# Optimization experiments

Hardware: AMD Instinct MI355X
Metric: run time of the kernel (lower is better)

Reference implementation:

```python
import jax, jax.numpy as jnp
import numpy as np

B = 16; Hp = 24; Wp = 24; N = Hp * Wp + 2  # 578 = patches + cls + freq tokens
D = 768; H = 12; HDIM = D // H
BAND = 64; SD = 16  # sd = min(16, max(4, band_dim))
HID = 3072  # int(embed_dim * mlp_ratio)
SCALE = HDIM ** -0.5; CLIP = 10.0
FILM_SCALE = 0.5; SPEC_INIT = 0.02; GATE_INIT = 0.05


def _ln(x, w, b, eps=1e-6):
    m = jnp.mean(x, axis=-1, keepdims=True)
    v = jnp.mean((x - m) ** 2, axis=-1, keepdims=True)
    return (x - m) * jax.lax.rsqrt(v + eps) * w + b


def _rms(x, eps=1e-6):
    return x * jax.lax.rsqrt(jnp.mean(x * x, axis=-1, keepdims=True) + eps)


def setup_inputs() -> dict:
    key = jax.random.key(0)
    ks = jax.random.split(key, 16)
    rn = lambda k, s, sc=1.0: jax.random.normal(k, s, dtype=jnp.float32) * sc
    return {
        "x": rn(ks[0], (B, N, D)),
        "band_tokens": rn(ks[1], (B, 1, D)),  # unused by forward (matches torch signature)
        "freq_token_for_cond": rn(ks[2], (B, 1, D)),
        "freq_summary": rn(ks[3], (B, D)),
        "token_band_feat": rn(ks[4], (B, N, BAND)),
        "alpha": jnp.ones((1,), jnp.float32),
        "ln_gate_w": jnp.ones((D,), jnp.float32), "ln_gate_b": jnp.zeros((D,), jnp.float32),
        "film_w": rn(ks[5], (D, 2 * D), 1e-4), "film_b": jnp.zeros((2 * D,), jnp.float32),
        "ln_attn_w": jnp.ones((D,), jnp.float32), "ln_attn_b": jnp.zeros((D,), jnp.float32),
        "qkv_w": rn(ks[6], (D, 3 * D), 0.02), "qkv_b": jnp.zeros((3 * D,), jnp.float32),
        "proj_w": rn(ks[7], (D, D), 0.02), "proj_b": jnp.zeros((D,), jnp.float32),
        "spec_bias_scale": jnp.float32(SPEC_INIT),
        "gate_w": rn(ks[8], (D, H), 1e-4), "gate_b": jnp.zeros((H,), jnp.float32),
        "band_proj_w": rn(ks[9], (BAND, SD), 0.02),
        "ln_mlp_w": jnp.ones((D,), jnp.float32), "ln_mlp_b": jnp.zeros((D,), jnp.float32),
        "fc1_w": rn(ks[10], (D, HID), 0.02), "fc1_b": jnp.zeros((HID,), jnp.float32),
        "fc2_w": rn(ks[11], (HID, D), 0.02), "fc2_b": jnp.zeros((D,), jnp.float32),
        "dw_w": rn(ks[12], (HID, 1, 3, 3), 0.1), "dw_b": jnp.zeros((HID,), jnp.float32),
    }


def _forward(x, band_tokens, freq_token_for_cond, freq_summary, token_band_feat, alpha,
             ln_gate_w, ln_gate_b, film_w, film_b, ln_attn_w, ln_attn_b,
             qkv_w, qkv_b, proj_w, proj_b, spec_bias_scale, gate_w, gate_b, band_proj_w,
             ln_mlp_w, ln_mlp_b, fc1_w, fc1_b, fc2_w, fc2_b, dw_w, dw_b):
    a = alpha.reshape(())
    # --- FiLM gate on patch tokens (replaces patch, no residual) ---
    cls_freq = x[:, :2]
    patch = x[:, 2:]
    p = _ln(patch, ln_gate_w, ln_gate_b)
    gb = freq_summary @ film_w + film_b            # [B, 2D]
    gamma, beta = jnp.split(gb, 2, axis=-1)
    gamma = jnp.tanh(gamma) * FILM_SCALE
    beta = jnp.tanh(beta) * FILM_SCALE
    patch = p * (1.0 + a * gamma[:, None, :]) + a * beta[:, None, :]
    x = jnp.concatenate([cls_freq, patch], axis=1)
    # --- spectral-similarity attention ---
    xn = _ln(x, ln_attn_w, ln_attn_b)
    qkv = (xn @ qkv_w + qkv_b).reshape(B, N, 3, H, HDIM)
    q = _rms(qkv[:, :, 0].transpose(0, 2, 1, 3))   # [B,H,N,hd]
    k = _rms(qkv[:, :, 1].transpose(0, 2, 1, 3))
    v = qkv[:, :, 2].transpose(0, 2, 1, 3)
    logits = jnp.einsum('bhnd,bhmd->bhnm', q * SCALE, k)
    s = _rms(token_band_feat @ band_proj_w)        # [B,N,SD]
    ssim = jnp.einsum('bns,bms->bnm', s, s)        # [B,N,N]
    logits = jnp.clip(logits + a * spec_bias_scale * ssim[:, None], -CLIP, CLIP)
    attn = jax.nn.softmax(logits, axis=-1)
    out = jnp.einsum('bhnm,bhmd->bhnd', attn, v)
    g = jnp.tanh(freq_token_for_cond[:, 0] @ gate_w + gate_b) * GATE_INIT  # [B,H]
    out = out * (1.0 + a * g[:, :, None, None])
    out = out.transpose(0, 2, 1, 3).reshape(B, N, D)
    x = x + (out @ proj_w + proj_b)
    # --- conv MLP on patch tokens only ---
    cls_freq = x[:, :2]
    patch = x[:, 2:]
    h = jax.nn.gelu(_ln(patch, ln_mlp_w, ln_mlp_b) @ fc1_w + fc1_b, approximate=False)
    h = h.transpose(0, 2, 1).reshape(B, HID, Hp, Wp)
    h = jax.lax.conv_general_dilated(h, dw_w, (1, 1), 'SAME', feature_group_count=HID,
                                     dimension_numbers=('NCHW', 'OIHW', 'NCHW'))
    h = jax.nn.silu(h + dw_b[None, :, None, None])
    h = h.reshape(B, HID, Hp * Wp).transpose(0, 2, 1)
    patch = patch + (h @ fc2_w + fc2_b)
    return jnp.concatenate([cls_freq, patch], axis=1)


def reference(x, band_tokens, freq_token_for_cond, freq_summary, token_band_feat, alpha,
              ln_gate_w, ln_gate_b, film_w, film_b, ln_attn_w, ln_attn_b,
              qkv_w, qkv_b, proj_w, proj_b, spec_bias_scale, gate_w, gate_b, band_proj_w,
              ln_mlp_w, ln_mlp_b, fc1_w, fc1_b, fc2_w, fc2_b, dw_w, dw_b):
    return _forward(x, band_tokens, freq_token_for_cond, freq_summary, token_band_feat, alpha,
                    ln_gate_w, ln_gate_b, film_w, film_b, ln_attn_w, ln_attn_b,
                    qkv_w, qkv_b, proj_w, proj_b, spec_bias_scale, gate_w, gate_b, band_proj_w,
                    ln_mlp_w, ln_mlp_b, fc1_w, fc1_b, fc2_w, fc2_b, dw_w, dw_b)
```

## Files before the change

### kernel.cpp

```cpp
#include <hip/hip_runtime.h>
#include <hip/hip_bf16.h>

#define BATCH 16
#define NTOK 578
#define NTOKP 592
#define NP 576
#define PGRID 24
#define DIM 768
#define NH 12
#define HDIM 64
#define BAND 64
#define SDIM 16
#define HID 3072
#define SCALE 0.125f
#define CLIPV 10.0f
#define KHS 104
#define VTS 72
#define PLS 72
#define FKS 16

typedef __attribute__((ext_vector_type(8))) short bf16x8;
typedef __attribute__((ext_vector_type(4))) float f32x4;

__device__ __forceinline__ float b2f(short u) {
  union { float f; unsigned int i; } x;
  x.i = ((unsigned int)(unsigned short)u) << 16;
  return x.f;
}
__device__ __forceinline__ short f2b(float x) {
  __hip_bfloat16 h = __float2bfloat16(x);
  return *reinterpret_cast<short*>(&h);
}

__device__ __forceinline__ void gload16(const short* g, short* l) {
  __builtin_amdgcn_global_load_lds(
      (const __attribute__((address_space(1))) unsigned int*)g,
      (__attribute__((address_space(3))) unsigned int*)l, 16, 0, 0);
}

__device__ __forceinline__ int swz_wgid(int orig, int nwg) {
  int xcd = orig & 7, i = orig >> 3;
  int q = nwg >> 3, r = nwg & 7;
  return (xcd < r) ? xcd * (q + 1) + i : r * (q + 1) + (xcd - r) * q + i;
}

__device__ __forceinline__ void block_reduce2(float& a, float& b) {
  __shared__ float sm[8];
  #pragma unroll
  for (int o = 32; o > 0; o >>= 1) { a += __shfl_down(a, o); b += __shfl_down(b, o); }
  int lane = threadIdx.x & 63, w = threadIdx.x >> 6;
  __syncthreads();
  if (lane == 0) { sm[w] = a; sm[4 + w] = b; }
  __syncthreads();
  a = sm[0] + sm[1] + sm[2] + sm[3];
  b = sm[4] + sm[5] + sm[6] + sm[7];
}

#define TKS 266
__device__ __forceinline__ void tw2(
    const float* __restrict__ W, short* __restrict__ Wt, int K, int N,
    int kblk, int nblk, short* t) {
  int tid = threadIdx.x;
  int k0 = kblk * 256, n0 = nblk * 64;
  int r0 = tid >> 4, c0 = (tid & 15) * 4;
  #pragma unroll
  for (int it = 0; it < 16; it++) {
    int r = it * 16 + r0;
    float4 v = *(const float4*)(W + (size_t)(k0 + r) * N + n0 + c0);
    t[(c0 + 0) * TKS + r] = f2b(v.x);
    t[(c0 + 1) * TKS + r] = f2b(v.y);
    t[(c0 + 2) * TKS + r] = f2b(v.z);
    t[(c0 + 3) * TKS + r] = f2b(v.w);
  }
  __syncthreads();
  int n1 = tid >> 5, k1 = (tid & 31) * 8;
  #pragma unroll
  for (int it = 0; it < 8; it++) {
    int n = it * 8 + n1;
    *(bf16x8*)(Wt + (size_t)(n0 + n) * K + k0 + k1) = *(bf16x8*)(t + n * TKS + k1);
  }
}

__global__ __launch_bounds__(256) void prep_weights(
    const float* __restrict__ qkv_w, const float* __restrict__ proj_w,
    const float* __restrict__ fc1_w, const float* __restrict__ fc2_w,
    const float* __restrict__ dww,
    short* __restrict__ qkvT, short* __restrict__ projT,
    short* __restrict__ fc1T, short* __restrict__ fc2T, float* __restrict__ dwt) {
  __shared__ short t[64 * TKS];
  int id = blockIdx.x;
  if (id < 108) {
    tw2(qkv_w, qkvT, 768, 2304, id % 3, id / 3, t);
  } else if (id < 144) {
    int u = id - 108; tw2(proj_w, projT, 768, 768, u % 3, u / 3, t);
  } else if (id < 288) {
    int u = id - 144; tw2(fc1_w, fc1T, 768, 3072, u % 3, u / 3, t);
  } else if (id < 432) {
    int u = id - 288; tw2(fc2_w, fc2T, 3072, 768, u % 12, u / 12, t);
  } else {
    int i = (id - 432) * 256 + threadIdx.x;
    if (i < 9 * HID) { int tt = i / HID, c = i - tt * HID; dwt[i] = dww[c * 9 + tt]; }
  }
}

__global__ __launch_bounds__(256) void film_part(
    const float* __restrict__ fsum, const float* __restrict__ film_w,
    float* __restrict__ part) {
  __shared__ float fs[BATCH][48];
  int bid = blockIdx.x;
  int cg = bid % 12, ks = bid / 12;
  int tid = threadIdx.x;
  int k0 = ks * 48;
  for (int i = tid; i < BATCH * 48; i += 256) {
    int b = i / 48, kk = i - b * 48;
    fs[b][kk] = fsum[b * DIM + k0 + kk];
  }
  __syncthreads();
  int col4 = cg * 128 + (tid & 31) * 4;
  int bq = tid >> 5;
  float a0[4] = {0.f, 0.f, 0.f, 0.f}, a1[4] = {0.f, 0.f, 0.f, 0.f};
  #pragma unroll 4
  for (int kk = 0; kk < 48; kk++) {
    float4 w = *(const float4*)(film_w + (size_t)(k0 + kk) * 2 * DIM + col4);
    float f0 = fs[bq][kk], f1 = fs[bq + 8][kk];
    a0[0] += f0 * w.x; a0[1] += f0 * w.y; a0[2] += f0 * w.z; a0[3] += f0 * w.w;
    a1[0] += f1 * w.x; a1[1] += f1 * w.y; a1[2] += f1 * w.z; a1[3] += f1 * w.w;
  }
  *(float4*)(part + ((size_t)ks * BATCH + bq) * 1536 + col4) =
      (float4){a0[0], a0[1], a0[2], a0[3]};
  *(float4*)(part + ((size_t)ks * BATCH + bq + 8) * 1536 + col4) =
      (float4){a1[0], a1[1], a1[2], a1[3]};
}

__global__ __launch_bounds__(256) void film_fin(
    const float* __restrict__ part, const float* __restrict__ film_b,
    const float* __restrict__ ftc, const float* __restrict__ gate_w,
    const float* __restrict__ gate_b,
    float* __restrict__ gamma, float* __restrict__ beta, float* __restrict__ g) {
  int bid = blockIdx.x;
  if (bid < 96) {
    int idx = bid * 256 + threadIdx.x;
    int b = idx / 1536, col = idx - b * 1536;
    float acc = film_b[col];
    #pragma unroll
    for (int ks = 0; ks < FKS; ks++)
      acc += part[((size_t)ks * BATCH + b) * 1536 + col];
    float t = tanhf(acc) * 0.5f;
    if (col < DIM) gamma[b * DIM + col] = t;
    else beta[b * DIM + (col - DIM)] = t;
  } else {
    int widx = (bid - 96) * 4 + (threadIdx.x >> 6);
    int lane = threadIdx.x & 63;
    if (widx < BATCH * NH) {
      int b = widx / NH, h = widx - b * NH;
      float acc = 0.f;
      for (int kk = lane; kk < DIM; kk += 64) acc += ftc[b * DIM + kk] * gate_w[kk * NH + h];
      #pragma unroll
      for (int o = 32; o > 0; o >>= 1) acc += __shfl_down(acc, o);
      if (lane == 0) g[widx] = tanhf(acc + gate_b[h]) * 0.05f;
    }
  }
}

__global__ __launch_bounds__(256) void band_s_kernel(
    const float* __restrict__ tbf, const float* __restrict__ bw, float* __restrict__ s) {
  int row = blockIdx.x * 4 + (threadIdx.x >> 6);
  int lane = threadIdx.x & 63;
  if (row >= BATCH * NTOK) return;
  const float* t = tbf + (size_t)row * BAND;
  float val = 0.f;
  if (lane < SDIM) {
    for (int i = 0; i < BAND; i++) val += t[i] * bw[i * SDIM + lane];
  }
  float ss = val * val;
  #pragma unroll
  for (int o = 8; o > 0; o >>= 1) ss += __shfl_xor(ss, o, 16);
  if (lane < SDIM) s[(size_t)row * SDIM + lane] = val * rsqrtf(ss * (1.f / 16.f) + 1e-6f);
}

__global__ __launch_bounds__(256) void transpose_v(
    const short* __restrict__ v, short* __restrict__ vT) {
  __shared__ short t[64][72];
  int bh = blockIdx.y;
  int n0 = blockIdx.x * 64;
  int tid = threadIdx.x;
  const short* vb = v + (size_t)bh * NTOK * HDIM;
  short* ob = vT + (size_t)bh * HDIM * NTOKP;
  {
    int r = tid >> 2, c0 = (tid & 3) * 16;
    int n = n0 + r;
    bf16x8 a0 = {0,0,0,0,0,0,0,0}, a1 = {0,0,0,0,0,0,0,0};
    if (n < NTOK) {
      a0 = *(const bf16x8*)(vb + (size_t)n * HDIM + c0);
      a1 = *(const bf16x8*)(vb + (size_t)n * HDIM + c0 + 8);
    }
    *(bf16x8*)(&t[r][c0]) = a0;
    *(bf16x8*)(&t[r][c0 + 8]) = a1;
  }
  __syncthreads();
  {
    int d = tid & 63, nc = tid >> 6;
    int nbase = n0 + nc * 16;
    short tmp[16];
    #pragma unroll
    for (int e = 0; e < 16; e++) tmp[e] = t[nc * 16 + e][d];
    if (nbase + 16 <= NTOK) {
      *(bf16x8*)(ob + (size_t)d * NTOKP + nbase) = *(bf16x8*)tmp;
      *(bf16x8*)(ob + (size_t)d * NTOKP + nbase + 8) = *(bf16x8*)(tmp + 8);
    } else {
      for (int e = 0; e < 16; e++)
        if (nbase + e < NTOK) ob[(size_t)d * NTOKP + nbase + e] = tmp[e];
    }
  }
}

__global__ __launch_bounds__(256) void ln_film_kernel(
    const float* __restrict__ x, const float* __restrict__ gamma, const float* __restrict__ beta,
    const float* __restrict__ gw, const float* __restrict__ gb,
    const float* __restrict__ aw, const float* __restrict__ ab,
    const float* __restrict__ alpha, float* __restrict__ xw, __hip_bfloat16* __restrict__ xn) {
  int row = blockIdx.x;
  int b = row / NTOK, n = row % NTOK;
  int tid = threadIdx.x;
  const float* xr = x + (size_t)row * DIM;
  float vals[3];
  #pragma unroll
  for (int j = 0; j < 3; j++) vals[j] = xr[tid + j * 256];
  if (n >= 2) {
    float s = vals[0] + vals[1] + vals[2];
    float ss = vals[0]*vals[0] + vals[1]*vals[1] + vals[2]*vals[2];
    block_reduce2(s, ss);
    float mean = s * (1.f / 768.f);
    float inv = rsqrtf(ss * (1.f / 768.f) - mean * mean + 1e-6f);
    float a = alpha[0];
    #pragma unroll
    for (int j = 0; j < 3; j++) {
      int d = tid + j * 256;
      float p = (vals[j] - mean) * inv * gw[d] + gb[d];
      vals[j] = p * (1.f + a * gamma[(size_t)b * DIM + d]) + a * beta[(size_t)b * DIM + d];
    }
  }
  float* xwr = xw + (size_t)row * DIM;
  #pragma unroll
  for (int j = 0; j < 3; j++) xwr[tid + j * 256] = vals[j];
  float s = vals[0] + vals[1] + vals[2];
  float ss = vals[0]*vals[0] + vals[1]*vals[1] + vals[2]*vals[2];
  block_reduce2(s, ss);
  float mean = s * (1.f / 768.f);
  float inv = rsqrtf(ss * (1.f / 768.f) - mean * mean + 1e-6f);
  __hip_bfloat16* xnr = xn + (size_t)row * DIM;
  #pragma unroll
  for (int j = 0; j < 3; j++) {
    int d = tid + j * 256;
    xnr[d] = __float2bfloat16((vals[j] - mean) * inv * aw[d] + ab[d]);
  }
}

__device__ __forceinline__ void stage_tile256(
    const short* __restrict__ A, const short* __restrict__ Wt, int K,
    int m0, int n0, int kt, short* Al, short* Bl, int wid, int lrow, int lcolsw) {
  #pragma unroll
  for (int it = 0; it < 4; it++) {
    int r0 = wid * 8 + it * 64;
    gload16(A + (size_t)(m0 + r0 + lrow) * K + kt + lcolsw, Al + r0 * 64);
  }
  #pragma unroll
  for (int it = 0; it < 2; it++) {
    int r0 = wid * 8 + it * 64;
    gload16(Wt + (size_t)(n0 + r0 + lrow) * K + kt + lcolsw, Bl + r0 * 64);
  }
}

__device__ __forceinline__ void compute_tile256(
    const short* Al, const short* Bl, f32x4 acc[4][4],
    int wr, int wc, int ln15, int kb) {
  int rx = ln15 & 7;
  #pragma unroll
  for (int kk = 0; kk < 2; kk++) {
    int csw = ((kk * 4 + kb) ^ rx) * 8;
    bf16x8 af[4], bfr[4];
    #pragma unroll
    for (int i = 0; i < 4; i++)
      af[i] = *(const bf16x8*)(Al + (wr * 64 + i * 16 + ln15) * 64 + csw);
    #pragma unroll
    for (int j = 0; j < 4; j++)
      bfr[j] = *(const bf16x8*)(Bl + (wc * 64 + j * 16 + ln15) * 64 + csw);
    #pragma unroll
    for (int i = 0; i < 4; i++)
      #pragma unroll
      for (int j = 0; j < 4; j++)
        acc[i][j] = __builtin_amdgcn_mfma_f32_16x16x32_bf16(af[i], bfr[j], acc[i][j], 0, 0, 0);
  }
}

__device__ __forceinline__ void mfma_core_256(
    const short* __restrict__ A, const short* __restrict__ Wt,
    int K, int m0, int n0, f32x4 acc[4][4], short* Al, short* Bl) {
  int tid = threadIdx.x, lane = tid & 63, wid = tid >> 6;
  int wr = wid >> 1, wc = wid & 1;
  int ln15 = lane & 15, kb = lane >> 4;
  int lrow = lane >> 3;
  int lcolsw = (((lane & 7) ^ lrow) & 7) * 8;
  #pragma unroll
  for (int i = 0; i < 4; i++)
    #pragma unroll
    for (int j = 0; j < 4; j++) acc[i][j] = (f32x4){0.f, 0.f, 0.f, 0.f};
  for (int kt = 0; kt < K; kt += 64) {
    stage_tile256(A, Wt, K, m0, n0, kt, Al, Bl, wid, lrow, lcolsw);
    __syncthreads();
    compute_tile256(Al, Bl, acc, wr, wc, ln15, kb);
    __syncthreads();
  }
}

__device__ __forceinline__ void stage_tile64(
    const short* __restrict__ A, const short* __restrict__ Wt, int K,
    int m0, int n0, int kt, short* Al, short* Bl, int wid, int lrow, int lcolsw) {
  #pragma unroll
  for (int it = 0; it < 2; it++) {
    int r0 = wid * 8 + it * 32;
    gload16(A + (size_t)(m0 + r0 + lrow) * K + kt + lcolsw, Al + r0 * 64);
  }
  #pragma unroll
  for (int it = 0; it < 4; it++) {
    int r0 = wid * 8 + it * 32;
    gload16(Wt + (size_t)(n0 + r0 + lrow) * K + kt + lcolsw, Bl + r0 * 64);
  }
}

__device__ __forceinline__ void compute_tile64(
    const short* Al, const short* Bl, f32x4 acc[4][2],
    int wid, int ln15, int kb) {
  int rx = ln15 & 7;
  #pragma unroll
  for (int kk = 0; kk < 2; kk++) {
    int csw = ((kk * 4 + kb) ^ rx) * 8;
    bf16x8 af[4], bfr[2];
    #pragma unroll
    for (int i = 0; i < 4; i++)
      af[i] = *(const bf16x8*)(Al + (i * 16 + ln15) * 64 + csw);
    #pragma unroll
    for (int j = 0; j < 2; j++)
      bfr[j] = *(const bf16x8*)(Bl + (wid * 32 + j * 16 + ln15) * 64 + csw);
    #pragma unroll
    for (int i = 0; i < 4; i++)
      #pragma unroll
      for (int j = 0; j < 2; j++)
        acc[i][j] = __builtin_amdgcn_mfma_f32_16x16x32_bf16(af[i], bfr[j], acc[i][j], 0, 0, 0);
  }
}

__device__ __forceinline__ void mfma_core_64(
    const short* __restrict__ A, const short* __restrict__ Wt,
    int K, int m0, int n0, f32x4 acc[4][2],
    short* Al0, short* Bl0, short* Al1, short* Bl1) {
  int tid = threadIdx.x, lane = tid & 63, wid = tid >> 6;
  int ln15 = lane & 15, kb = lane >> 4;
  int lrow = lane >> 3;
  int lcolsw = (((lane & 7) ^ lrow) & 7) * 8;
  #pragma unroll
  for (int i = 0; i < 4; i++)
    #pragma unroll
    for (int j = 0; j < 2; j++) acc[i][j] = (f32x4){0.f, 0.f, 0.f, 0.f};
  stage_tile64(A, Wt, K, m0, n0, 0, Al0, Bl0, wid, lrow, lcolsw);
  __syncthreads();
  for (int kt = 0; kt < K; kt += 128) {
    if (kt + 64 < K)
      stage_tile64(A, Wt, K, m0, n0, kt + 64, Al1, Bl1, wid, lrow, lcolsw);
    compute_tile64(Al0, Bl0, acc, wid, ln15, kb);
    __syncthreads();
    if (kt + 128 < K)
      stage_tile64(A, Wt, K, m0, n0, kt + 128, Al0, Bl0, wid, lrow, lcolsw);
    if (kt + 64 < K)
      compute_tile64(Al1, Bl1, acc, wid, ln15, kb);
    __syncthreads();
  }
}

__global__ __launch_bounds__(512) void gemm_qkv(
    const short* __restrict__ A, const short* __restrict__ Wt, const float* __restrict__ bias,
    __hip_bfloat16* __restrict__ q, __hip_bfloat16* __restrict__ k, __hip_bfloat16* __restrict__ v) {
  __shared__ short Al[256 * 64], Bl[128 * 64];
  f32x4 acc[4][4];
  int wgid = swz_wgid(blockIdx.x, 37 * 18);
  int m0 = (wgid % 37) * 256, n0 = (wgid / 37) * 128;
  mfma_core_256(A, Wt, DIM, m0, n0, acc, Al, Bl);
  int tid = threadIdx.x, lane = tid & 63, wid = tid >> 6, wr = wid >> 1, wc = wid & 1;
  int ln15 = lane & 15, lq = lane >> 4;
  int colbase = n0 + wc * 64;
  int which = colbase / DIM;
  int rem = colbase - which * DIM;
  int h = rem >> 6;
  __hip_bfloat16* dst = (which == 0) ? q : ((which == 1) ? k : v);
  float fin_scale = (which == 0) ? SCALE : 1.0f;
  float bv[4];
  #pragma unroll
  for (int j = 0; j < 4; j++) bv[j] = bias[colbase + j * 16 + ln15];
  #pragma unroll
  for (int i = 0; i < 4; i++) {
    #pragma unroll
    for (int r = 0; r < 4; r++) {
      int m = m0 + wr * 64 + i * 16 + lq * 4 + r;
      float v4[4];
      #pragma unroll
      for (int j = 0; j < 4; j++) v4[j] = acc[i][j][r] + bv[j];
      float inv = fin_scale;
      if (which < 2) {
        float ss = v4[0]*v4[0] + v4[1]*v4[1] + v4[2]*v4[2] + v4[3]*v4[3];
        ss += __shfl_xor(ss, 1); ss += __shfl_xor(ss, 2);
        ss += __shfl_xor(ss, 4); ss += __shfl_xor(ss, 8);
        inv = rsqrtf(ss * (1.f / 64.f) + 1e-6f) * fin_scale;
      }
      if (m < BATCH * NTOK) {
        int b = m / NTOK, n = m - b * NTOK;
        __hip_bfloat16* orow = dst + (((size_t)b * NH + h) * NTOK + n) * HDIM;
        #pragma unroll
        for (int j = 0; j < 4; j++)
          orow[j * 16 + ln15] = __float2bfloat16(v4[j] * inv);
      }
    }
  }
}

__global__ __launch_bounds__(512) void attn_mfma(
    const short* __restrict__ q, const short* __restrict__ k,
    const short* __restrict__ vT, const float* __restrict__ s,
    const float* __restrict__ g, const float* __restrict__ alpha,
    const float* __restrict__ sbs, short* __restrict__ ao) {
  __shared__ short Kh[2][64 * KHS];
  __shared__ short Vt[2][64 * VTS];
  __shared__ short Pl[8][16 * PLS];
  int xcd = blockIdx.x & 7, idx = blockIdx.x >> 3;
  int bh = xcd * 24 + idx / 5;
  int n0 = (idx % 5) * 128;
  int b = bh / NH, h = bh - b * NH;
  int tid = threadIdx.x, lane = tid & 63, w = tid >> 6;
  int l15 = lane & 15, lg = lane >> 4;
  float a = alpha[0], c = a * sbs[0];
  const short* qb = q + (size_t)bh * NTOK * HDIM;
  const short* kb = k + (size_t)bh * NTOK * HDIM;
  const short* vtb = vT + (size_t)bh * HDIM * NTOKP;
  const float* sb = s + (size_t)b * NTOK * SDIM;
  const bf16x8 Z8 = {0, 0, 0, 0, 0, 0, 0, 0};

  int qrow = n0 + w * 16 + l15;
  int qsrc = (qrow < NTOK) ? qrow : 0;
  bf16x8 qf0 = *(const bf16x8*)(qb + (size_t)qsrc * HDIM + lg * 8);
  bf16x8 qf1 = *(const bf16x8*)(qb + (size_t)qsrc * HDIM + 32 + lg * 8);
  bf16x8 qf2 = Z8;
  if (lg < 2) {
    const float* sp = sb + (size_t)qsrc * SDIM + lg * 8;
    #pragma unroll
    for (int j = 0; j < 8; j++) qf2[j] = f2b(c * sp[j]);
  }

  f32x4 accO[4];
  #pragma unroll
  for (int dd = 0; dd < 4; dd++) accO[dd] = (f32x4){0.f, 0.f, 0.f, 0.f};
  float rsum[4] = {0.f, 0.f, 0.f, 0.f};

  int srow = (tid & 255) >> 2, sseg = tid & 3;
  if (tid < 256 && sseg == 3) {
    #pragma unroll
    for (int bb = 0; bb < 2; bb++) {
      short* dst = Kh[bb] + srow * KHS + 80;
      *(bf16x8*)dst = Z8;
      *(bf16x8*)(dst + 8) = Z8;
    }
  }

  auto stage = [&](int mt, short* KhB, short* VtB) {
    if (tid < 256) {
      int key = mt + srow;
      bool kok = key < NTOK;
      if (sseg < 2) {
        bf16x8 v0 = Z8, v1 = Z8, v2 = Z8, v3 = Z8;
        if (kok) {
          const short* src = kb + (size_t)key * HDIM + sseg * 32;
          v0 = *(const bf16x8*)(src);
          v1 = *(const bf16x8*)(src + 8);
          v2 = *(const bf16x8*)(src + 16);
          v3 = *(const bf16x8*)(src + 24);
        }
        short* dst = KhB + srow * KHS + sseg * 32;
        *(bf16x8*)dst = v0;
        *(bf16x8*)(dst + 8) = v1;
        *(bf16x8*)(dst + 16) = v2;
        *(bf16x8*)(dst + 24) = v3;
      } else if (sseg == 2) {
        bf16x8 v0 = Z8, v1 = Z8;
        if (kok) {
          const float* sp = sb + (size_t)key * SDIM;
          #pragma unroll
          for (int j = 0; j < 8; j++) { v0[j] = f2b(sp[j]); v1[j] = f2b(sp[j + 8]); }
        }
        short* dst = KhB + srow * KHS + 64;
        *(bf16x8*)dst = v0;
        *(bf16x8*)(dst + 8) = v1;
      }
    } else {
      int kk0 = sseg * 16;
      short* dst = VtB + srow * VTS + kk0;
      const short* src = vtb + (size_t)srow * NTOKP + mt + kk0;
      if (mt + kk0 + 16 <= NTOK) {
        *(bf16x8*)dst = *(const bf16x8*)src;
        *(bf16x8*)(dst + 8) = *(const bf16x8*)(src + 8);
      } else {
        for (int e = 0; e < 16; e++)
          dst[e] = (mt + kk0 + e < NTOK) ? src[e] : (short)0;
      }
    }
  };

  stage(0, Kh[0], Vt[0]);
  __syncthreads();
  const int NT = 10;
  for (int ti = 0; ti < NT; ti++) {
    int mt = ti * 64, cur = ti & 1;
    if (ti + 1 < NT) stage(mt + 64, Kh[cur ^ 1], Vt[cur ^ 1]);
    const short* KhC = Kh[cur];
    const short* VtC = Vt[cur];
    f32x4 sa[4];
    __builtin_amdgcn_s_setprio(1);
    #pragma unroll
    for (int jj = 0; jj < 4; jj++) {
      sa[jj] = (f32x4){0.f, 0.f, 0.f, 0.f};
      const short* kp = KhC + (jj * 16 + l15) * KHS + lg * 8;
      sa[jj] = __builtin_amdgcn_mfma_f32_16x16x32_bf16(qf0, *(const bf16x8*)kp, sa[jj], 0, 0, 0);
      sa[jj] = __builtin_amdgcn_mfma_f32_16x16x32_bf16(qf1, *(const bf16x8*)(kp + 32), sa[jj], 0, 0, 0);
      sa[jj] = __builtin_amdgcn_mfma_f32_16x16x32_bf16(qf2, *(const bf16x8*)(kp + 64), sa[jj], 0, 0, 0);
    }
    __builtin_amdgcn_s_setprio(0);
    short* pw = Pl[w];
    float ps[4][4];
    #pragma unroll
    for (int jj = 0; jj < 4; jj++) {
      bool ok = (mt + jj * 16 + l15) < NTOK;
      #pragma unroll
      for (int r = 0; r < 4; r++) {
        float x = sa[jj][r];
        x = fminf(fmaxf(x, -CLIPV), CLIPV);
        float e = ok ? __expf(x) : 0.f;
        ps[jj][r] = e;
        pw[(lg * 4 + r) * PLS + jj * 16 + l15] = f2b(e);
      }
    }
    #pragma unroll
    for (int r = 0; r < 4; r++) {
      float t = ps[0][r] + ps[1][r] + ps[2][r] + ps[3][r];
      t += __shfl_xor(t, 1); t += __shfl_xor(t, 2);
      t += __shfl_xor(t, 4); t += __shfl_xor(t, 8);
      rsum[r] += t;
    }
    __builtin_amdgcn_s_setprio(1);
    #pragma unroll
    for (int kc = 0; kc < 2; kc++) {
      bf16x8 pa = *(const bf16x8*)(pw + l15 * PLS + kc * 32 + lg * 8);
      #pragma unroll
      for (int dd = 0; dd < 4; dd++) {
        bf16x8 vf = *(const bf16x8*)(VtC + (dd * 16 + l15) * VTS + kc * 32 + lg * 8);
        accO[dd] = __builtin_amdgcn_mfma_f32_16x16x32_bf16(pa, vf, accO[dd], 0, 0, 0);
      }
    }
    __builtin_amdgcn_s_setprio(0);
    __syncthreads();
  }
  float gm = 1.f + a * g[bh];
  #pragma unroll
  for (int r = 0; r < 4; r++) {
    int n = n0 + w * 16 + lg * 4 + r;
    if (n >= NTOK) continue;
    float inv = gm / rsum[r];
    short* orow = ao + ((size_t)b * NTOK + n) * DIM + h * HDIM;
    #pragma unroll
    for (int dd = 0; dd < 4; dd++)
      orow[dd * 16 + l15] = f2b(accO[dd][r] * inv);
  }
}

__global__ __launch_bounds__(256) void gemm_proj(
    const short* __restrict__ A, const short* __restrict__ Wt, const float* __restrict__ bias,
    float* __restrict__ xw, float* __restrict__ out) {
  __shared__ short Al0[64 * 64], Bl0[128 * 64], Al1[64 * 64], Bl1[128 * 64];
  f32x4 acc[4][2];
  int wgid = swz_wgid(blockIdx.x, 145 * 6);
  int m0 = (wgid % 145) * 64, n0 = (wgid / 145) * 128;
  mfma_core_64(A, Wt, DIM, m0, n0, acc, Al0, Bl0, Al1, Bl1);
  int tid = threadIdx.x, lane = tid & 63, wid = tid >> 6;
  int ln15 = lane & 15, lq = lane >> 4;
  #pragma unroll
  for (int i = 0; i < 4; i++) {
    #pragma unroll
    for (int j = 0; j < 2; j++) {
      int col = n0 + wid * 32 + j * 16 + ln15;
      float bv = bias[col];
      #pragma unroll
      for (int r = 0; r < 4; r++) {
        int m = m0 + i * 16 + lq * 4 + r;
        if (m >= BATCH * NTOK) continue;
        int n = m % NTOK;
        float val = acc[i][j][r] + bv + xw[(size_t)m * DIM + col];
        xw[(size_t)m * DIM + col] = val;
        if (n < 2) out[(size_t)m * DIM + col] = val;
      }
    }
  }
}

__global__ __launch_bounds__(256) void ln_mlp_kernel(
    const float* __restrict__ x2, const float* __restrict__ w, const float* __restrict__ bb,
    __hip_bfloat16* __restrict__ xm) {
  int r = blockIdx.x;
  int b = r / NP, pi = r % NP;
  int tid = threadIdx.x;
  const float* xr = x2 + ((size_t)b * NTOK + 2 + pi) * DIM;
  float vals[3];
  #pragma unroll
  for (int j = 0; j < 3; j++) vals[j] = xr[tid + j * 256];
  float s = vals[0] + vals[1] + vals[2];
  float ss = vals[0]*vals[0] + vals[1]*vals[1] + vals[2]*vals[2];
  block_reduce2(s, ss);
  float mean = s * (1.f / 768.f);
  float inv = rsqrtf(ss * (1.f / 768.f) - mean * mean + 1e-6f);
  __hip_bfloat16* xo = xm + (size_t)r * DIM;
  #pragma unroll
  for (int j = 0; j < 3; j++) {
    int d = tid + j * 256;
    xo[d] = __float2bfloat16((vals[j] - mean) * inv * w[d] + bb[d]);
  }
}

__global__ __launch_bounds__(512) void gemm_fc1(
    const short* __restrict__ A, const short* __restrict__ Wt, const float* __restrict__ bias,
    __hip_bfloat16* __restrict__ h1) {
  __shared__ short Al[256 * 64], Bl[128 * 64];
  f32x4 acc[4][4];
  int wgid = swz_wgid(blockIdx.x, 18 * 24);
  int m0 = (wgid % 18) * 256, n0 = (wgid / 18) * 128;
  mfma_core_256(A, Wt, DIM, m0, n0, acc, Al, Bl);
  int tid = threadIdx.x, lane = tid & 63, wid = tid >> 6, wr = wid >> 1, wc = wid & 1;
  int ln15 = lane & 15, lq = lane >> 4;
  #pragma unroll
  for (int i = 0; i < 4; i++) {
    #pragma unroll
    for (int j = 0; j < 4; j++) {
      int col = n0 + wc * 64 + j * 16 + ln15;
      float bv = bias[col];
      #pragma unroll
      for (int r = 0; r < 4; r++) {
        int m = m0 + wr * 64 + i * 16 + lq * 4 + r;
        float val = acc[i][j][r] + bv;
        float ge = 0.5f * val * (1.f + erff(val * 0.70710678118f));
        h1[(size_t)m * HID + col] = __float2bfloat16(ge);
      }
    }
  }
}

__global__ __launch_bounds__(256) void dwconv_kernel(
    const __hip_bfloat16* __restrict__ h1, const float* __restrict__ dwt,
    const float* __restrict__ dwb, __hip_bfloat16* __restrict__ h2) {
  int gx = blockIdx.x;
  int b = gx / 144, g = gx - b * 144;
  int y = g / 6, x0 = (g - y * 6) * 4;
  int tid = threadIdx.x;
  int c0 = blockIdx.y * 512 + (tid & 63) * 8;
  int x = x0 + (tid >> 6);
  const short* in = (const short*)h1 + (size_t)b * NP * HID + c0;
  bf16x8 iv[3][3];
  #pragma unroll
  for (int ky = 0; ky < 3; ky++) {
    int yy = y + ky - 1;
    #pragma unroll
    for (int kx = 0; kx < 3; kx++) {
      int xx = x + kx - 1;
      bool ok = (yy >= 0 && yy < PGRID && xx >= 0 && xx < PGRID);
      iv[ky][kx] = ok ? *(const bf16x8*)(in + (size_t)(yy * PGRID + xx) * HID)
                      : (bf16x8){0, 0, 0, 0, 0, 0, 0, 0};
    }
  }
  float acc[8];
  {
    float4 b0 = *(const float4*)(dwb + c0);
    float4 b1 = *(const float4*)(dwb + c0 + 4);
    acc[0] = b0.x; acc[1] = b0.y; acc[2] = b0.z; acc[3] = b0.w;
    acc[4] = b1.x; acc[5] = b1.y; acc[6] = b1.z; acc[7] = b1.w;
  }
  #pragma unroll
  for (int t = 0; t < 9; t++) {
    float4 w0 = *(const float4*)(dwt + t * HID + c0);
    float4 w1 = *(const float4*)(dwt + t * HID + c0 + 4);
    bf16x8 xv = iv[t / 3][t % 3];
    acc[0] += b2f(xv[0]) * w0.x; acc[1] += b2f(xv[1]) * w0.y;
    acc[2] += b2f(xv[2]) * w0.z; acc[3] += b2f(xv[3]) * w0.w;
    acc[4] += b2f(xv[4]) * w1.x; acc[5] += b2f(xv[5]) * w1.y;
    acc[6] += b2f(xv[6]) * w1.z; acc[7] += b2f(xv[7]) * w1.w;
  }
  short ov[8];
  #pragma unroll
  for (int e = 0; e < 8; e++) {
    float v = acc[e];
    ov[e] = f2b(v / (1.f + __expf(-v)));
  }
  *(bf16x8*)((short*)h2 + ((size_t)b * NP + y * PGRID + x) * HID + c0) = *(bf16x8*)ov;
}

__global__ __launch_bounds__(256) void gemm_fc2(
    const short* __restrict__ A, const short* __restrict__ Wt, const float* __restrict__ bias,
    const float* __restrict__ xw, float* __restrict__ out, int b0) {
  __shared__ short Al0[64 * 64], Bl0[128 * 64], Al1[64 * 64], Bl1[128 * 64];
  f32x4 acc[4][2];
  int wgid = swz_wgid(blockIdx.x, 72 * 6);
  int m0 = (wgid % 72) * 64, n0 = (wgid / 72) * 128;
  mfma_core_64(A, Wt, HID, m0, n0, acc, Al0, Bl0, Al1, Bl1);
  int tid = threadIdx.x, lane = tid & 63, wid = tid >> 6;
  int ln15 = lane & 15, lq = lane >> 4;
  #pragma unroll
  for (int i = 0; i < 4; i++) {
    #pragma unroll
    for (int j = 0; j < 2; j++) {
      int col = n0 + wid * 32 + j * 16 + ln15;
      float bv = bias[col];
      #pragma unroll
      for (int r = 0; r < 4; r++) {
        int m = m0 + i * 16 + lq * 4 + r;
        int bl = m / NP, pi = m - bl * NP;
        size_t orow = ((size_t)(b0 + bl) * NTOK + 2 + pi) * DIM;
        out[orow + col] = acc[i][j][r] + bv + xw[orow + col];
      }
    }
  }
}

extern "C" void kernel_launch(void* const* d_in, const int* in_sizes, int n_in,
                              void* d_out, int out_size, void* d_ws, size_t ws_size,
                              hipStream_t stream) {
  const float* x      = (const float*)d_in[0];
  const float* ftc    = (const float*)d_in[2];
  const float* fsum   = (const float*)d_in[3];
  const float* tbf    = (const float*)d_in[4];
  const float* alpha  = (const float*)d_in[5];
  const float* lgw    = (const float*)d_in[6];
  const float* lgb    = (const float*)d_in[7];
  const float* film_w = (const float*)d_in[8];
  const float* film_b = (const float*)d_in[9];
  const float* law    = (const float*)d_in[10];
  const float* lab    = (const float*)d_in[11];
  const float* qkv_w  = (const float*)d_in[12];
  const float* qkv_b  = (const float*)d_in[13];
  const float* proj_w = (const float*)d_in[14];
  const float* proj_b = (const float*)d_in[15];
  const float* sbs    = (const float*)d_in[16];
  const float* gate_w = (const float*)d_in[17];
  const float* gate_b = (const float*)d_in[18];
  const float* band_w = (const float*)d_in[19];
  const float* lmw    = (const float*)d_in[20];
  const float* lmb    = (const float*)d_in[21];
  const float* fc1_w  = (const float*)d_in[22];
  const float* fc1_b  = (const float*)d_in[23];
  const float* fc2_w  = (const float*)d_in[24];
  const float* fc2_b  = (const float*)d_in[25];
  const float* dw_w   = (const float*)d_in[26];
  const float* dw_b   = (const float*)d_in[27];
  float* out = (float*)d_out;

  float* ws = (float*)d_ws;
  const size_t SZ = (size_t)BATCH * NTOK * DIM;

  float* p_xw = ws;
  short* p_xn = (short*)(ws + SZ);
  short* p_q  = (short*)(ws + SZ + SZ / 2);
  short* p_k  = (short*)(ws + 2 * SZ);
  short* p_v  = (short*)(ws + 2 * SZ + SZ / 2);
  float* p_s  = ws + 3 * SZ;
  float* p_gamma = p_s + (size_t)BATCH * NTOK * SDIM;
  float* p_beta  = p_gamma + BATCH * DIM;
  float* p_g     = p_beta + BATCH * DIM;
  float* p_dwt   = p_g + 256;
  float* p_part  = p_dwt + 9 * HID;
  float* wtb = p_part + (size_t)FKS * BATCH * 1536;
  short* qkvT = (short*)wtb;
  short* projT = qkvT + (size_t)768 * 2304;
  short* fc1T  = projT + (size_t)768 * 768;
  short* fc2T  = fc1T + (size_t)768 * 3072;
  short* h2c   = fc2T + (size_t)3072 * 768;

  const size_t total_floats =
      3 * SZ + (size_t)BATCH * NTOK * SDIM + 2 * (size_t)BATCH * DIM + 256 + 9 * HID +
      (size_t)FKS * BATCH * 1536 +
      ((size_t)768 * 2304 + 768 * 768 + 768 * 3072 + 3072 * 768) / 2 +
      ((size_t)8 * NP * HID) / 2;
  if (ws_size < total_floats * sizeof(float)) return;

  short* p_ao = p_xn;
  short* p_xm = p_q;
  short* h1c  = p_k;
  short* p_vT = h2c;

  dim3 blk(256);

  prep_weights<<<dim3(432 + 108), blk, 0, stream>>>(
      qkv_w, proj_w, fc1_w, fc2_w, dw_w, qkvT, projT, fc1T, fc2T, p_dwt);

  film_part<<<dim3(12 * FKS), blk, 0, stream>>>(fsum, film_w, p_part);

  film_fin<<<dim3(96 + 48), blk, 0, stream>>>(
      p_part, film_b, ftc, gate_w, gate_b, p_gamma, p_beta, p_g);

  band_s_kernel<<<dim3((BATCH * NTOK + 3) / 4), blk, 0, stream>>>(tbf, band_w, p_s);

  ln_film_kernel<<<dim3(BATCH * NTOK), blk, 0, stream>>>(
      x, p_gamma, p_beta, lgw, lgb, law, lab, alpha, p_xw, (__hip_bfloat16*)p_xn);

  gemm_qkv<<<dim3(37 * 18), dim3(512), 0, stream>>>(
      p_xn, qkvT, qkv_b, (__hip_bfloat16*)p_q, (__hip_bfloat16*)p_k, (__hip_bfloat16*)p_v);

  transpose_v<<<dim3(10, BATCH * NH), blk, 0, stream>>>(p_v, p_vT);

  attn_mfma<<<dim3(960), dim3(512), 0, stream>>>(
      p_q, p_k, p_vT, p_s, p_g, alpha, sbs, p_ao);

  gemm_proj<<<dim3(145 * 6), blk, 0, stream>>>(p_ao, projT, proj_b, p_xw, out);

  ln_mlp_kernel<<<dim3(BATCH * NP), blk, 0, stream>>>(p_xw, lmw, lmb, (__hip_bfloat16*)p_xm);

  for (int cc = 0; cc < 2; cc++) {
    const short* Ach = p_xm + (size_t)cc * 4608 * DIM;
    gemm_fc1<<<dim3(18 * 24), dim3(512), 0, stream>>>(Ach, fc1T, fc1_b, (__hip_bfloat16*)h1c);
    dwconv_kernel<<<dim3(8 * 144, 6), blk, 0, stream>>>(
        (const __hip_bfloat16*)h1c, p_dwt, dw_b, (__hip_bfloat16*)h2c);
    gemm_fc2<<<dim3(72 * 6), blk, 0, stream>>>(h2c, fc2T, fc2_b, p_xw, out, cc * 8);
  }
}
```

Measured before the change: 440.8 us.

## Pipeline 64-wide GEMM loads with vmcnt waits and single-buffer attention K tile

The 64-tile GEMM core now prefetches two K-tiles ahead. It uses raw s_barrier plus explicit s_waitcnt vmcnt counts instead of full __syncthreads, so global loads stay in flight across the barrier. The attention kernel drops the double-buffered K tile and uses one K buffer. A barrier is added after the QK MFMAs, after which the next K/V tile is staged, which lowers LDS use and may raise occupancy. The risks are that the hand-counted vmcnt values may not match the loads the compiler actually emits, and the extra barrier in attention serializes K staging against the score computation.

```diff
diff --git a/kernel.cpp b/kernel.cpp
--- a/kernel.cpp
+++ b/kernel.cpp
@@ -363,17 +363,24 @@
     #pragma unroll
     for (int j = 0; j < 2; j++) acc[i][j] = (f32x4){0.f, 0.f, 0.f, 0.f};
   stage_tile64(A, Wt, K, m0, n0, 0, Al0, Bl0, wid, lrow, lcolsw);
-  __syncthreads();
-  for (int kt = 0; kt < K; kt += 128) {
-    if (kt + 64 < K)
-      stage_tile64(A, Wt, K, m0, n0, kt + 64, Al1, Bl1, wid, lrow, lcolsw);
-    compute_tile64(Al0, Bl0, acc, wid, ln15, kb);
-    __syncthreads();
-    if (kt + 128 < K)
-      stage_tile64(A, Wt, K, m0, n0, kt + 128, Al0, Bl0, wid, lrow, lcolsw);
-    if (kt + 64 < K)
-      compute_tile64(Al1, Bl1, acc, wid, ln15, kb);
-    __syncthreads();
+  stage_tile64(A, Wt, K, m0, n0, 64, Al1, Bl1, wid, lrow, lcolsw);
+  asm volatile("s_waitcnt vmcnt(6)" ::: "memory");
+  __builtin_amdgcn_s_barrier();
+  const int NKT = K >> 6;
+  for (int t = 0; t < NKT; t++) {
+    const short* Ac = (t & 1) ? Al1 : Al0;
+    const short* Bc = (t & 1) ? Bl1 : Bl0;
+    compute_tile64(Ac, Bc, acc, wid, ln15, kb);
+    __builtin_amdgcn_s_barrier();
+    if (t + 2 < NKT) {
+      short* As = (t & 1) ? Al1 : Al0;
+      short* Bs = (t & 1) ? Bl1 : Bl0;
+      stage_tile64(A, Wt, K, m0, n0, (t + 2) << 6, As, Bs, wid, lrow, lcolsw);
+      asm volatile("s_waitcnt vmcnt(6)" ::: "memory");
+    } else if (t + 1 < NKT) {
+      asm volatile("s_waitcnt vmcnt(0)" ::: "memory");
+    }
+    __builtin_amdgcn_s_barrier();
   }
 }
 
@@ -427,7 +434,7 @@
     const short* __restrict__ vT, const float* __restrict__ s,
     const float* __restrict__ g, const float* __restrict__ alpha,
     const float* __restrict__ sbs, short* __restrict__ ao) {
-  __shared__ short Kh[2][64 * KHS];
+  __shared__ short Kh[64 * KHS];
   __shared__ short Vt[2][64 * VTS];
   __shared__ short Pl[8][16 * PLS];
   int xcd = blockIdx.x & 7, idx = blockIdx.x >> 3;
@@ -461,76 +468,75 @@
 
   int srow = (tid & 255) >> 2, sseg = tid & 3;
   if (tid < 256 && sseg == 3) {
-    #pragma unroll
-    for (int bb = 0; bb < 2; bb++) {
-      short* dst = Kh[bb] + srow * KHS + 80;
-      *(bf16x8*)dst = Z8;
-      *(bf16x8*)(dst + 8) = Z8;
-    }
-  }
-
-  auto stage = [&](int mt, short* KhB, short* VtB) {
-    if (tid < 256) {
-      int key = mt + srow;
-      bool kok = key < NTOK;
-      if (sseg < 2) {
-        bf16x8 v0 = Z8, v1 = Z8, v2 = Z8, v3 = Z8;
-        if (kok) {
-          const short* src = kb + (size_t)key * HDIM + sseg * 32;
-          v0 = *(const bf16x8*)(src);
-          v1 = *(const bf16x8*)(src + 8);
-          v2 = *(const bf16x8*)(src + 16);
-          v3 = *(const bf16x8*)(src + 24);
-        }
-        short* dst = KhB + srow * KHS + sseg * 32;
-        *(bf16x8*)dst = v0;
-        *(bf16x8*)(dst + 8) = v1;
-        *(bf16x8*)(dst + 16) = v2;
-        *(bf16x8*)(dst + 24) = v3;
-      } else if (sseg == 2) {
-        bf16x8 v0 = Z8, v1 = Z8;
-        if (kok) {
-          const float* sp = sb + (size_t)key * SDIM;
-          #pragma unroll
-          for (int j = 0; j < 8; j++) { v0[j] = f2b(sp[j]); v1[j] = f2b(sp[j + 8]); }
-        }
-        short* dst = KhB + srow * KHS + 64;
-        *(bf16x8*)dst = v0;
-        *(bf16x8*)(dst + 8) = v1;
+    short* dst = Kh + srow * KHS + 80;
+    *(bf16x8*)dst = Z8;
+    *(bf16x8*)(dst + 8) = Z8;
+  }
+
+  auto stageK = [&](int mt) {
+    int key = mt + srow;
+    bool kok = key < NTOK;
+    if (sseg < 2) {
+      bf16x8 v0 = Z8, v1 = Z8, v2 = Z8, v3 = Z8;
+      if (kok) {
+        const short* src = kb + (size_t)key * HDIM + sseg * 32;
+        v0 = *(const bf16x8*)(src);
+        v1 = *(const bf16x8*)(src + 8);
+        v2 = *(const bf16x8*)(src + 16);
+        v3 = *(const bf16x8*)(src + 24);
       }
+      short* dst = Kh + srow * KHS + sseg * 32;
+      *(bf16x8*)dst = v0;
+      *(bf16x8*)(dst + 8) = v1;
+      *(bf16x8*)(dst + 16) = v2;
+      *(bf16x8*)(dst + 24) = v3;
+    } else if (sseg == 2) {
+      bf16x8 v0 = Z8, v1 = Z8;
+      if (kok) {
+        const float* sp = sb + (size_t)key * SDIM;
+        #pragma unroll
+        for (int j = 0; j < 8; j++) { v0[j] = f2b(sp[j]); v1[j] = f2b(sp[j + 8]); }
+      }
+      short* dst = Kh + srow * KHS + 64;
+      *(bf16x8*)dst = v0;
+      *(bf16x8*)(dst + 8) = v1;
+    }
+  };
+  auto stageV = [&](int mt, short* VtB) {
+    int kk0 = sseg * 16;
+    short* dst = VtB + srow * VTS + kk0;
+    const short* src = vtb + (size_t)srow * NTOKP + mt + kk0;
+    if (mt + kk0 + 16 <= NTOK) {
+      *(bf16x8*)dst = *(const bf16x8*)src;
+      *(bf16x8*)(dst + 8) = *(const bf16x8*)(src + 8);
     } else {
-      int kk0 = sseg * 16;
-      short* dst = VtB + srow * VTS + kk0;
-      const short* src = vtb + (size_t)srow * NTOKP + mt + kk0;
-      if (mt + kk0 + 16 <= NTOK) {
-        *(bf16x8*)dst = *(const bf16x8*)src;
-        *(bf16x8*)(dst + 8) = *(const bf16x8*)(src + 8);
-      } else {
-        for (int e = 0; e < 16; e++)
-          dst[e] = (mt + kk0 + e < NTOK) ? src[e] : (short)0;
-      }
+      for (int e = 0; e < 16; e++)
+        dst[e] = (mt + kk0 + e < NTOK) ? src[e] : (short)0;
     }
   };
 
-  stage(0, Kh[0], Vt[0]);
+  if (tid < 256) stageK(0); else stageV(0, Vt[0]);
   __syncthreads();
   const int NT = 10;
   for (int ti = 0; ti < NT; ti++) {
     int mt = ti * 64, cur = ti & 1;
-    if (ti + 1 < NT) stage(mt + 64, Kh[cur ^ 1], Vt[cur ^ 1]);
-    const short* KhC = Kh[cur];
     const short* VtC = Vt[cur];
     f32x4 sa[4];
     __builtin_amdgcn_s_setprio(1);
     #pragma unroll
     for (int jj = 0; jj < 4; jj++) {
       sa[jj] = (f32x4){0.f, 0.f, 0.f, 0.f};
-      const short* kp = KhC + (jj * 16 + l15) * KHS + lg * 8;
+      const short* kp = Kh + (jj * 16 + l15) * KHS + lg * 8;
       sa[jj] = __builtin_amdgcn_mfma_f32_16x16x32_bf16(qf0, *(const bf16x8*)kp, sa[jj], 0, 0, 0);
       sa[jj] = __builtin_amdgcn_mfma_f32_16x16x32_bf16(qf1, *(const bf16x8*)(kp + 32), sa[jj], 0, 0, 0);
       sa[jj] = __builtin_amdgcn_mfma_f32_16x16x32_bf16(qf2, *(const bf16x8*)(kp + 64), sa[jj], 0, 0, 0);
     }
     __builtin_amdgcn_s_setprio(0);
+    __syncthreads();
+    if (ti + 1 < NT) {
+      if (tid < 256) stageK(mt + 64);
+      else stageV(mt + 64, Vt[cur ^ 1]);
+    }
     short* pw = Pl[w];
     float ps[4][4];
     #pragma unroll
```

Result: no change. 443.5 us (+0.6%).
